# Optimization experiments

Hardware: AMD Instinct MI355X
Metric: run time of the kernel (lower is better)

## Reference

```python
import jax, jax.numpy as jnp
import numpy as np

N_EMBD = 768
N_HEAD = 12
HEAD_DIM = N_EMBD // N_HEAD


def setup_inputs() -> dict:
    key = jax.random.key(0)
    k0, k1, k2, k3, k4 = jax.random.split(key, 5)
    B, T, C = 2, 4096, N_EMBD
    x = jax.random.normal(k0, (B, T, C), dtype=jnp.float32)
    # c_attn: Linear(C, 3C); c_proj: Linear(C, C). torch Linear: y = x @ W.T + b
    s = 1.0 / np.sqrt(C)
    W_attn = jax.random.uniform(k1, (3 * C, C), dtype=jnp.float32, minval=-s, maxval=s)
    b_attn = jax.random.uniform(k2, (3 * C,), dtype=jnp.float32, minval=-s, maxval=s)
    W_proj = jax.random.uniform(k3, (C, C), dtype=jnp.float32, minval=-s, maxval=s)
    b_proj = jax.random.uniform(k4, (C,), dtype=jnp.float32, minval=-s, maxval=s)
    return {"x": x, "W_attn": W_attn, "b_attn": b_attn, "W_proj": W_proj, "b_proj": b_proj}


def reference(x, W_attn, b_attn, W_proj, b_proj):
    B, T, C = x.shape
    H, D = N_HEAD, HEAD_DIM
    qkv = x @ W_attn.T + b_attn                      # [B,T,3C]
    q, k, v = jnp.split(qkv, 3, axis=-1)
    # [B,T,C] -> [B,H,T,D]
    q = q.reshape(B, T, H, D).transpose(0, 2, 1, 3)
    k = k.reshape(B, T, H, D).transpose(0, 2, 1, 3)
    v = v.reshape(B, T, H, D).transpose(0, 2, 1, 3)
    scale = 1.0 / jnp.sqrt(jnp.asarray(D, dtype=x.dtype))
    att = jnp.einsum('bhqd,bhkd->bhqk', q, k) * scale  # [B,H,T,T]
    att = jax.nn.softmax(att, axis=-1)
    y = jnp.einsum('bhqk,bhkd->bhqd', att, v)          # [B,H,T,D]
    y = y.transpose(0, 2, 1, 3).reshape(B, T, C)
    return y @ W_proj.T + b_proj
```

## Files before the change

### kernel.cpp

```cpp
#include <hip/hip_runtime.h>
#include <stdint.h>
#include <stddef.h>

typedef __bf16 bf16_t;
typedef bf16_t bf16x4 __attribute__((ext_vector_type(4)));
typedef bf16_t bf16x8 __attribute__((ext_vector_type(8)));
typedef float  f32x4  __attribute__((ext_vector_type(4)));
typedef _Float16 f16_t;
typedef f16_t f16x2 __attribute__((ext_vector_type(2)));
typedef f16_t f16x4 __attribute__((ext_vector_type(4)));
typedef __fp16 fp16x2_raw __attribute__((ext_vector_type(2)));

__device__ __forceinline__ f16x2 pkrtz(float a, float b) {
    fp16x2_raw r = __builtin_amdgcn_cvt_pkrtz(a, b);
    union { fp16x2_raw r; f16x2 h; } u;
    u.r = r;
    return u.h;
}

#define MFMA_BF16_K32(a, b, c) __builtin_amdgcn_mfma_f32_16x16x32_bf16(a, b, c, 0, 0, 0)
#define MFMA_F16_K16(a, b, c)  __builtin_amdgcn_mfma_f32_16x16x16f16(a, b, c, 0, 0, 0)

__device__ __forceinline__ void gload_lds16(const void* g, void* l) {
    __builtin_amdgcn_global_load_lds(
        (const __attribute__((address_space(1))) void*)g,
        (__attribute__((address_space(3))) void*)l,
        16, 0, 0);
}

#define NX 1572864
#define NWA 442368
#define NWP 147456
__global__ void cvt_all(const float* __restrict__ x, const float* __restrict__ Wa,
                        const float* __restrict__ Wp, bf16_t* __restrict__ xb,
                        bf16_t* __restrict__ Wab, bf16_t* __restrict__ Wpb) {
    int i = blockIdx.x * blockDim.x + threadIdx.x;
    const float4* src; bf16_t* dst; int j;
    if (i < NX)            { src = (const float4*)x;  dst = xb;  j = i; }
    else if (i < NX + NWA) { src = (const float4*)Wa; dst = Wab; j = i - NX; }
    else                   { src = (const float4*)Wp; dst = Wpb; j = i - NX - NWA; }
    float4 f = src[j];
    bf16x4 o = { (bf16_t)f.x, (bf16_t)f.y, (bf16_t)f.z, (bf16_t)f.w };
    ((bf16x4*)dst)[j] = o;
}

template <int KDIM>
__device__ __forceinline__ void gemm_mainloop(
    const bf16_t* __restrict__ A, const bf16_t* __restrict__ Bt,
    bf16_t* As, bf16_t* Bs, int m0, int n0, int wave, int lane, f32x4 acc[4][4])
{
    const int quad = lane >> 4, l15 = lane & 15;
    const int wm = ((wave >> 1) << 6), wn = ((wave & 1) << 6);

    const int srow = (wave << 4) + (lane >> 2);
    const int sw   = (((lane & 3) ^ ((srow >> 1) & 3)) << 3);
    const bf16_t* gA = A  + (size_t)(m0 + srow) * KDIM + sw;
    const bf16_t* gB = Bt + (size_t)(n0 + srow) * KDIM + sw;
    bf16_t* lA0 = As + wave * 512;
    bf16_t* lA1 = As + 2048 + wave * 512;
    bf16_t* lB0 = Bs + wave * 512;
    bf16_t* lB1 = Bs + 2048 + wave * 512;

    const int xorv = ((quad ^ ((l15 >> 1) & 3)) << 3);

    for (int k0 = 0; k0 < KDIM; k0 += 32) {
        __syncthreads();
        gload_lds16(gA + k0,                       lA0);
        gload_lds16(gA + (size_t)64 * KDIM + k0,   lA1);
        gload_lds16(gB + k0,                       lB0);
        gload_lds16(gB + (size_t)64 * KDIM + k0,   lB1);
        __syncthreads();

        bf16x8 af[4], bfr[4];
#pragma unroll
        for (int t = 0; t < 4; t++) {
            af[t]  = *(const bf16x8*)(As + (wm + t * 16 + l15) * 32 + xorv);
            bfr[t] = *(const bf16x8*)(Bs + (wn + t * 16 + l15) * 32 + xorv);
        }
#pragma unroll
        for (int mt = 0; mt < 4; mt++)
#pragma unroll
            for (int nt = 0; nt < 4; nt++)
                acc[mt][nt] = MFMA_BF16_K32(af[mt], bfr[nt], acc[mt][nt]);
    }
}

__global__ __launch_bounds__(256) void gemm_qkv(
    const bf16_t* __restrict__ Wab,
    const bf16_t* __restrict__ xb,
    const float* __restrict__ bias,
    bf16_t* __restrict__ qo, bf16_t* __restrict__ ko, f16_t* __restrict__ vo)
{
    __shared__ bf16_t As[128 * 32];
    __shared__ bf16_t Bs[128 * 32];
    const int tid = threadIdx.x, wave = tid >> 6, lane = tid & 63;
    const int quad = lane >> 4, l15 = lane & 15;
    const int m0 = blockIdx.x * 128;
    const int n0 = blockIdx.y * 128;
    f32x4 acc[4][4] = {};
    gemm_mainloop<768>(Wab, xb, As, Bs, m0, n0, wave, lane, acc);

    const int wm = ((wave >> 1) << 6), wn = ((wave & 1) << 6);
#pragma unroll
    for (int nt = 0; nt < 4; nt++) {
        const int tok = n0 + wn + nt * 16 + l15;
        const int b = tok >> 12, tt = tok & 4095;
#pragma unroll
        for (int mt = 0; mt < 4; mt++) {
            const int f0 = m0 + wm + mt * 16 + quad * 4;
            const float4 bi = *(const float4*)(bias + f0);
            const int which = f0 / 768;
            const int rem = f0 - which * 768;
            const int h = rem >> 6, d0 = rem & 63;
            const float v0 = acc[mt][nt][0] + bi.x, v1 = acc[mt][nt][1] + bi.y;
            const float v2 = acc[mt][nt][2] + bi.z, v3 = acc[mt][nt][3] + bi.w;
            if (which < 2) {
                bf16_t* dst = (which == 0) ? qo : ko;
                bf16x4 ov = { (bf16_t)v0, (bf16_t)v1, (bf16_t)v2, (bf16_t)v3 };
                *(bf16x4*)(dst + ((size_t)(b * 12 + h) * 4096 + tt) * 64 + d0) = ov;
            } else {
                f16_t* vd = vo + ((size_t)(b * 12 + h) * 64 + d0) * 4096 + tt;
                vd[0]         = (f16_t)v0;
                vd[4096]      = (f16_t)v1;
                vd[2 * 4096]  = (f16_t)v2;
                vd[3 * 4096]  = (f16_t)v3;
            }
        }
    }
}

__global__ __launch_bounds__(256) void gemm_proj(
    const bf16_t* __restrict__ Wpb,
    const bf16_t* __restrict__ yb,
    const float* __restrict__ bias,
    float* __restrict__ out)
{
    __shared__ bf16_t As[128 * 32];
    __shared__ bf16_t Bs[128 * 32];
    const int tid = threadIdx.x, wave = tid >> 6, lane = tid & 63;
    const int quad = lane >> 4, l15 = lane & 15;
    const int m0 = blockIdx.x * 128;
    const int n0 = blockIdx.y * 128;
    f32x4 acc[4][4] = {};
    gemm_mainloop<768>(Wpb, yb, As, Bs, m0, n0, wave, lane, acc);

    const int wm = ((wave >> 1) << 6), wn = ((wave & 1) << 6);
#pragma unroll
    for (int nt = 0; nt < 4; nt++) {
        const int tok = n0 + wn + nt * 16 + l15;
#pragma unroll
        for (int mt = 0; mt < 4; mt++) {
            const int f0 = m0 + wm + mt * 16 + quad * 4;
            const float4 bi = *(const float4*)(bias + f0);
            float4 o = { acc[mt][nt][0] + bi.x, acc[mt][nt][1] + bi.y,
                         acc[mt][nt][2] + bi.z, acc[mt][nt][3] + bi.w };
            *(float4*)(out + (size_t)tok * 768 + f0) = o;
        }
    }
}

#define QSCALE 0.1803368801f
#define WAIT_VM4 0x0F74
#define WAIT_VM0 0x0F70
__global__ __launch_bounds__(256, 3) void attn_fwd(
    const bf16_t* __restrict__ qg, const bf16_t* __restrict__ kg,
    const f16_t* __restrict__ vtg, bf16_t* __restrict__ y)
{
    __shared__ __align__(16) bf16_t K0s[4096], K1s[4096], K2s[4096];
    __shared__ __align__(16) f16_t  V0s[4096], V1s[4096], V2s[4096];
    __shared__ __align__(16) float  Psr[256];
    __shared__ float PsT[64];
    float* RedA = (float*)K0s;
    float* RedB = (float*)(((char*)K0s) + 17408);

    const int tid = threadIdx.x, wave = tid >> 6, lane = tid & 63;
    const int quad = lane >> 4, l15 = lane & 15;

    const int blk = blockIdx.x;
    const int xcd = blk & 7;
    const int idx = blk >> 3;
    const int hl  = idx % 3;
    const int qt  = idx / 3;
    const int bh  = xcd * 3 + hl;
    const int b = bh / 12, h = bh - b * 12;
    const size_t base = (size_t)bh * 4096 * 64;
    const bf16_t* kgt = kg + base;
    const f16_t*  vgt = vtg + base;

    bf16x8 qf[4][2];
#pragma unroll
    for (int qc = 0; qc < 4; qc++) {
        const int qrow = qt * 64 + qc * 16 + l15;
        qf[qc][0] = *(const bf16x8*)(qg + base + (size_t)qrow * 64 + quad * 8);
        qf[qc][1] = *(const bf16x8*)(qg + base + (size_t)qrow * 64 + 32 + quad * 8);
#pragma unroll
        for (int j = 0; j < 8; j++) {
            qf[qc][0][j] = (bf16_t)((float)qf[qc][0][j] * QSCALE);
            qf[qc][1][j] = (bf16_t)((float)qf[qc][1][j] * QSCALE);
        }
    }

    f32x4 O[4][4] = {};
    float psum[4] = {};
    const f16x2 one2 = { (f16_t)1.0f, (f16_t)1.0f };

    const int srow8 = tid >> 3;
    const int sc8   = (tid & 7) ^ (srow8 & 7);
    const int l8 = l15 & 7;
    const int w16 = wave << 4;
    const int ksoff = (quad ^ l8) << 3;
    const int vslot = ((wave << 1) | (quad >> 1)) ^ l8;
    const int q0off = (quad & 1) * 8;

    auto stageT = [&](int t, bf16_t* Kd, f16_t* Vd) {
        const bf16_t* kp = kgt + (size_t)t * 4096;
        const f16_t*  vp = vgt + t * 64;
#pragma unroll
        for (int i = 0; i < 2; i++) {
            gload_lds16(kp + (i * 32 + srow8) * 64 + sc8 * 8,           Kd + (i * 256 + tid) * 8);
            gload_lds16(vp + (size_t)(i * 32 + srow8) * 4096 + sc8 * 8, Vd + (i * 256 + tid) * 8);
        }
    };

    auto compute = [&](const bf16_t* ks, const f16_t* vs) {
        const bf16_t* kr = ks + (w16 + l15) * 64;
        bf16x8 kf0 = *(const bf16x8*)(kr + ksoff);
        bf16x8 kf1 = *(const bf16x8*)(kr + (ksoff ^ 32));
        f32x4 sc[4];
#pragma unroll
        for (int qc = 0; qc < 4; qc++) {
            f32x4 s = {};
            s = MFMA_BF16_K32(kf0, qf[qc][0], s);
            s = MFMA_BF16_K32(kf1, qf[qc][1], s);
            sc[qc] = s;
        }
        f16x4 pf[4];
#pragma unroll
        for (int qc = 0; qc < 4; qc++) {
            float e0 = __builtin_amdgcn_exp2f(sc[qc][0]);
            float e1 = __builtin_amdgcn_exp2f(sc[qc][1]);
            float e2 = __builtin_amdgcn_exp2f(sc[qc][2]);
            float e3 = __builtin_amdgcn_exp2f(sc[qc][3]);
            f16x2 lo = pkrtz(e0, e1);
            f16x2 hi = pkrtz(e2, e3);
            psum[qc] = __builtin_amdgcn_fdot2(lo, one2, psum[qc], false);
            psum[qc] = __builtin_amdgcn_fdot2(hi, one2, psum[qc], false);
            f16x4 p;
            *(f16x2*)&p = lo;
            *(((f16x2*)&p) + 1) = hi;
            pf[qc] = p;
        }
#pragma unroll
        for (int dt = 0; dt < 4; dt++) {
            const char* vr = (const char*)(vs + (dt * 16 + l15) * 64);
            f16x4 vf = *(const f16x4*)(vr + vslot * 16 + q0off);
#pragma unroll
            for (int qc = 0; qc < 4; qc++)
                O[dt][qc] = MFMA_F16_K16(vf, pf[qc], O[dt][qc]);
        }
    };

    stageT(0, K0s, V0s);
    stageT(1, K1s, V1s);
    for (int t = 0; t < 63; t += 3) {
        __builtin_amdgcn_s_waitcnt(WAIT_VM4);
        __builtin_amdgcn_s_barrier();
        compute(K0s, V0s);
        stageT(t + 2, K2s, V2s);

        __builtin_amdgcn_s_waitcnt(WAIT_VM4);
        __builtin_amdgcn_s_barrier();
        compute(K1s, V1s);
        stageT(t + 3, K0s, V0s);

        __builtin_amdgcn_s_waitcnt(WAIT_VM4);
        __builtin_amdgcn_s_barrier();
        compute(K2s, V2s);
        stageT(t + 4 < 64 ? t + 4 : 63, K1s, V1s);
    }
    __builtin_amdgcn_s_waitcnt(WAIT_VM0);
    __builtin_amdgcn_s_barrier();
    compute(K0s, V0s);

#pragma unroll
    for (int qc = 0; qc < 4; qc++) {
        psum[qc] += __shfl_xor(psum[qc], 16, 64);
        psum[qc] += __shfl_xor(psum[qc], 32, 64);
    }
    __syncthreads();
    if (wave == 2) {
#pragma unroll
        for (int dt = 0; dt < 4; dt++)
#pragma unroll
            for (int qc = 0; qc < 4; qc++)
                *(f32x4*)(RedA + (qc * 16 + l15) * 68 + dt * 16 + quad * 4) = O[dt][qc];
    } else if (wave == 3) {
#pragma unroll
        for (int dt = 0; dt < 4; dt++)
#pragma unroll
            for (int qc = 0; qc < 4; qc++)
                *(f32x4*)(RedB + (qc * 16 + l15) * 68 + dt * 16 + quad * 4) = O[dt][qc];
    }
    if (quad == 0) {
#pragma unroll
        for (int qc = 0; qc < 4; qc++) Psr[wave * 64 + qc * 16 + l15] = psum[qc];
    }
    __syncthreads();
    if (wave == 0) {
#pragma unroll
        for (int dt = 0; dt < 4; dt++)
#pragma unroll
            for (int qc = 0; qc < 4; qc++)
                O[dt][qc] += *(const f32x4*)(RedA + (qc * 16 + l15) * 68 + dt * 16 + quad * 4);
    } else if (wave == 1) {
#pragma unroll
        for (int dt = 0; dt < 4; dt++)
#pragma unroll
            for (int qc = 0; qc < 4; qc++)
                O[dt][qc] += *(const f32x4*)(RedB + (qc * 16 + l15) * 68 + dt * 16 + quad * 4);
    }
    __syncthreads();
    if (wave == 1) {
#pragma unroll
        for (int dt = 0; dt < 4; dt++)
#pragma unroll
            for (int qc = 0; qc < 4; qc++)
                *(f32x4*)(RedA + (qc * 16 + l15) * 68 + dt * 16 + quad * 4) = O[dt][qc];
    } else if (wave == 3) {
        PsT[lane] = Psr[lane] + Psr[64 + lane] + Psr[128 + lane] + Psr[192 + lane];
    }
    __syncthreads();
    if (wave == 0) {
#pragma unroll
        for (int qc = 0; qc < 4; qc++) {
            const float rcp = 1.0f / PsT[qc * 16 + l15];
            const int t = qt * 64 + qc * 16 + l15;
            bf16_t* yr = y + ((size_t)b * 4096 + t) * 768 + h * 64 + quad * 4;
#pragma unroll
            for (int dt = 0; dt < 4; dt++) {
                f32x4 o4 = O[dt][qc] +
                    *(const f32x4*)(RedA + (qc * 16 + l15) * 68 + dt * 16 + quad * 4);
                bf16x4 ov = { (bf16_t)(o4[0] * rcp), (bf16_t)(o4[1] * rcp),
                              (bf16_t)(o4[2] * rcp), (bf16_t)(o4[3] * rcp) };
                *(bf16x4*)(yr + dt * 16) = ov;
            }
        }
    }
}

extern "C" void kernel_launch(void* const* d_in, const int* in_sizes, int n_in,
                              void* d_out, int out_size, void* d_ws, size_t ws_size,
                              hipStream_t stream) {
    const float* x  = (const float*)d_in[0];
    const float* Wa = (const float*)d_in[1];
    const float* ba = (const float*)d_in[2];
    const float* Wp = (const float*)d_in[3];
    const float* bp = (const float*)d_in[4];
    float* out = (float*)d_out;

    char* ws = (char*)d_ws;
    bf16_t* xb  = (bf16_t*)(ws);
    bf16_t* Wab = (bf16_t*)(ws + 12582912);
    bf16_t* Wpb = (bf16_t*)(ws + 16121856);
    bf16_t* qb  = (bf16_t*)(ws + 17301504);
    bf16_t* kb  = (bf16_t*)(ws + 29884416);
    f16_t*  vtb = (f16_t*)(ws + 42467328);
    bf16_t* yb  = (bf16_t*)(ws + 55050240);

    cvt_all<<<8448, 256, 0, stream>>>(x, Wa, Wp, xb, Wab, Wpb);
    gemm_qkv <<<dim3(18, 64), 256, 0, stream>>>(Wab, xb, ba, qb, kb, vtb);
    attn_fwd <<<1536, 256, 0, stream>>>(qb, kb, vtb, yb);
    gemm_proj<<<dim3( 6, 64), 256, 0, stream>>>(Wpb, yb, bp, out);
}
```

Baseline: 300.8 us.

## Give each wave private double-buffered K/V LDS tiles and drop block barriers

Each wave now stages only the 16 keys and matching V columns it consumes into its own private LDS region, double-buffered. This removes the per-tile workgroup s_barrier, since no wave depends on another wave's loads. The shared triple buffer is replaced by one smaller aliased shared array, which lowers LDS use and may allow more resident blocks. The trade-off is a shallower prefetch depth of two tiles instead of three. It also relies on in-wave ordering between LDS reads and the following async global-to-LDS writes into the same buffer.

Result: no change. 297.7 us (-1.0%).

```diff
diff --git a/kernel.cpp b/kernel.cpp
--- a/kernel.cpp
+++ b/kernel.cpp
@@ -166,12 +166,11 @@
     const bf16_t* __restrict__ qg, const bf16_t* __restrict__ kg,
     const f16_t* __restrict__ vtg, bf16_t* __restrict__ y)
 {
-    __shared__ __align__(16) bf16_t K0s[4096], K1s[4096], K2s[4096];
-    __shared__ __align__(16) f16_t  V0s[4096], V1s[4096], V2s[4096];
-    __shared__ __align__(16) float  Psr[256];
-    __shared__ float PsT[64];
-    float* RedA = (float*)K0s;
-    float* RedB = (float*)(((char*)K0s) + 17408);
+    __shared__ __align__(16) char smem[36864];
+    float* RedA = (float*)smem;
+    float* RedB = (float*)(smem + 17408);
+    float* Psr  = (float*)(smem + 34816);
+    float* PsT  = (float*)(smem + 35840);
 
     const int tid = threadIdx.x, wave = tid >> 6, lane = tid & 63;
     const int quad = lane >> 4, l15 = lane & 15;
@@ -187,6 +186,12 @@
     const bf16_t* kgt = kg + base;
     const f16_t*  vgt = vtg + base;
 
+    char* wbase = smem + wave * 8192;
+    bf16_t* K0w = (bf16_t*)(wbase);
+    f16_t*  V0w = (f16_t*)(wbase + 2048);
+    bf16_t* K1w = (bf16_t*)(wbase + 4096);
+    f16_t*  V1w = (f16_t*)(wbase + 6144);
+
     bf16x8 qf[4][2];
 #pragma unroll
     for (int qc = 0; qc < 4; qc++) {
@@ -204,26 +209,25 @@
     float psum[4] = {};
     const f16x2 one2 = { (f16_t)1.0f, (f16_t)1.0f };
 
-    const int srow8 = tid >> 3;
-    const int sc8   = (tid & 7) ^ (srow8 & 7);
     const int l8 = l15 & 7;
     const int w16 = wave << 4;
     const int ksoff = (quad ^ l8) << 3;
-    const int vslot = ((wave << 1) | (quad >> 1)) ^ l8;
-    const int q0off = (quad & 1) * 8;
+    const int krow = lane >> 3;
+    const int kchk = (lane & 7) ^ krow;
+    const int vrow = lane >> 1;
+    const int vhalf = (lane & 1) << 3;
 
     auto stageT = [&](int t, bf16_t* Kd, f16_t* Vd) {
-        const bf16_t* kp = kgt + (size_t)t * 4096;
-        const f16_t*  vp = vgt + t * 64;
-#pragma unroll
-        for (int i = 0; i < 2; i++) {
-            gload_lds16(kp + (i * 32 + srow8) * 64 + sc8 * 8,           Kd + (i * 256 + tid) * 8);
-            gload_lds16(vp + (size_t)(i * 32 + srow8) * 4096 + sc8 * 8, Vd + (i * 256 + tid) * 8);
-        }
+        const bf16_t* kp = kgt + (size_t)(t * 64 + w16) * 64;
+        const f16_t*  vp = vgt + t * 64 + w16;
+        gload_lds16(kp + krow * 64 + kchk * 8,               Kd);
+        gload_lds16(kp + (8 + krow) * 64 + kchk * 8,         Kd + 512);
+        gload_lds16(vp + (size_t)vrow * 4096 + vhalf,        Vd);
+        gload_lds16(vp + (size_t)(32 + vrow) * 4096 + vhalf, Vd + 512);
     };
 
     auto compute = [&](const bf16_t* ks, const f16_t* vs) {
-        const bf16_t* kr = ks + (w16 + l15) * 64;
+        const bf16_t* kr = ks + l15 * 64;
         bf16x8 kf0 = *(const bf16x8*)(kr + ksoff);
         bf16x8 kf1 = *(const bf16x8*)(kr + (ksoff ^ 32));
         f32x4 sc[4];
@@ -252,35 +256,28 @@
         }
 #pragma unroll
         for (int dt = 0; dt < 4; dt++) {
-            const char* vr = (const char*)(vs + (dt * 16 + l15) * 64);
-            f16x4 vf = *(const f16x4*)(vr + vslot * 16 + q0off);
+            f16x4 vf = *(const f16x4*)(vs + (dt * 16 + l15) * 16 + quad * 4);
 #pragma unroll
             for (int qc = 0; qc < 4; qc++)
                 O[dt][qc] = MFMA_F16_K16(vf, pf[qc], O[dt][qc]);
         }
     };
 
-    stageT(0, K0s, V0s);
-    stageT(1, K1s, V1s);
-    for (int t = 0; t < 63; t += 3) {
+    __builtin_amdgcn_s_waitcnt(WAIT_VM0);
+    stageT(0, K0w, V0w);
+    stageT(1, K1w, V1w);
+    for (int t = 0; t < 62; t += 2) {
         __builtin_amdgcn_s_waitcnt(WAIT_VM4);
-        __builtin_amdgcn_s_barrier();
-        compute(K0s, V0s);
-        stageT(t + 2, K2s, V2s);
-
+        compute(K0w, V0w);
+        stageT(t + 2, K0w, V0w);
         __builtin_amdgcn_s_waitcnt(WAIT_VM4);
-        __builtin_amdgcn_s_barrier();
-        compute(K1s, V1s);
-        stageT(t + 3, K0s, V0s);
-
-        __builtin_amdgcn_s_waitcnt(WAIT_VM4);
-        __builtin_amdgcn_s_barrier();
-        compute(K2s, V2s);
-        stageT(t + 4 < 64 ? t + 4 : 63, K1s, V1s);
-    }
+        compute(K1w, V1w);
+        stageT(t + 3, K1w, V1w);
+    }
+    __builtin_amdgcn_s_waitcnt(WAIT_VM4);
+    compute(K0w, V0w);
     __builtin_amdgcn_s_waitcnt(WAIT_VM0);
-    __builtin_amdgcn_s_barrier();
-    compute(K0s, V0s);
+    compute(K1w, V1w);
 
 #pragma unroll
     for (int qc = 0; qc < 4; qc++) {
```
